# Kernel tuning notes

Measured on AMD Instinct MI355X. Metric: run time of the kernel, lower is better.

## Reference

```python
import jax, jax.numpy as jnp
import numpy as np

M = 16384      # total flat points per role (8 scenes x 2048 pts)
D = 256        # d_model
H = 4          # heads
K = 16         # knn neighbors
DFF = 1024     # 4*D
LN_EPS = 1e-5


def _ln(x, g, b):
    m = jnp.mean(x, axis=-1, keepdims=True)
    v = jnp.mean((x - m) ** 2, axis=-1, keepdims=True)
    return (x - m) / jnp.sqrt(v + LN_EPS) * g + b


def _knn_block(x, coord, ctx, ctx_coord, idx,
               Wq, Wk, Wv, Wo, g1, b1, pe_w, pe_b,
               W1, bf1, W2, bf2, g2, b2):
    # x: [M,D] query feats; ctx: [N,D] context feats; idx: [M,K] neighbor ids (-1 = invalid)
    m, d = x.shape
    k = idx.shape[1]
    dh = d // H
    valid = idx >= 0
    idx_c = jnp.where(valid, idx, 0)

    xn = _ln(x, g1, b1)
    q = (xn @ Wq).reshape(m, H, dh)                      # [M,H,dh]
    k_all = ctx @ Wk                                     # [N,D]
    v_all = ctx @ Wv                                     # [N,D]

    rel = coord[:, None, :] - ctx_coord[idx_c]           # [M,K,3]
    pe = rel @ pe_w + pe_b                               # [M,K,D] relative position encoding
    kg = (k_all[idx_c] + pe).reshape(m, k, H, dh)        # gathered keys  [M,K,H,dh]
    vg = (v_all[idx_c] + pe).reshape(m, k, H, dh)        # gathered values

    scale = jnp.asarray(1.0 / np.sqrt(dh), x.dtype)
    scores = jnp.einsum('mhd,mkhd->mhk', q, kg) * scale
    scores = jnp.where(valid[:, None, :], scores, jnp.asarray(-1e9, x.dtype))
    attn = jax.nn.softmax(scores, axis=-1)
    out = jnp.einsum('mhk,mkhd->mhd', attn, vg).reshape(m, d) @ Wo
    x = x + out
    h = jax.nn.gelu(_ln(x, g2, b2) @ W1 + bf1)
    return x + (h @ W2 + bf2)


def setup_inputs() -> dict:
    key = jax.random.key(0)
    ks = jax.random.split(key, 24)
    s = 0.02
    nblk = 2  # [0]=self(a), [1]=cross(a,b)
    inp = {
        'feat_a': jax.random.normal(ks[0], (M, D), jnp.float32),
        'coord_a': jax.random.normal(ks[1], (M, 3), jnp.float32),
        'feat_b': jax.random.normal(ks[2], (M, D), jnp.float32),
        'coord_b': jax.random.normal(ks[3], (M, 3), jnp.float32),
        'Wq': jax.random.normal(ks[4], (nblk, D, D), jnp.float32) * s,
        'Wk': jax.random.normal(ks[5], (nblk, D, D), jnp.float32) * s,
        'Wv': jax.random.normal(ks[6], (nblk, D, D), jnp.float32) * s,
        'Wo': jax.random.normal(ks[7], (nblk, D, D), jnp.float32) * s,
        'ln1_g': jnp.ones((nblk, D), jnp.float32),
        'ln1_b': jnp.zeros((nblk, D), jnp.float32),
        'pe_w': jax.random.normal(ks[8], (nblk, 3, D), jnp.float32) * s,
        'pe_b': jnp.zeros((nblk, D), jnp.float32),
        'ffn_w1': jax.random.normal(ks[9], (nblk, D, DFF), jnp.float32) * s,
        'ffn_b1': jnp.zeros((nblk, DFF), jnp.float32),
        'ffn_w2': jax.random.normal(ks[10], (nblk, DFF, D), jnp.float32) * s,
        'ffn_b2': jnp.zeros((nblk, D), jnp.float32),
        'ln2_g': jnp.ones((nblk, D), jnp.float32),
        'ln2_b': jnp.zeros((nblk, D), jnp.float32),
        'knn_a2a': jax.random.randint(ks[11], (M, K), 0, M, jnp.int64 if jax.config.jax_enable_x64 else jnp.int32),
        'knn_a2b': jax.random.randint(ks[12], (M, K), 0, M, jnp.int64 if jax.config.jax_enable_x64 else jnp.int32),
    }
    return inp


def reference(feat_a, coord_a, feat_b, coord_b,
              Wq, Wk, Wv, Wo, ln1_g, ln1_b, pe_w, pe_b,
              ffn_w1, ffn_b1, ffn_w2, ffn_b2, ln2_g, ln2_b,
              knn_a2a, knn_a2b):
    def params(i):
        return (Wq[i], Wk[i], Wv[i], Wo[i], ln1_g[i], ln1_b[i], pe_w[i], pe_b[i],
                ffn_w1[i], ffn_b1[i], ffn_w2[i], ffn_b2[i], ln2_g[i], ln2_b[i])
    # layer 'self(a)': feat[a] = block(feat[a], coord[a], knn_indexes['a2a'])
    fa = _knn_block(feat_a, coord_a, feat_a, coord_a, knn_a2a, *params(0))
    # layer 'cross(a,b)': feat[a] = block(query=feat[a], context=feat[b], knn_indexes['a2b'])
    fa = _knn_block(fa, coord_a, feat_b, coord_b, knn_a2b, *params(1))
    return fa
```

## Files before the change

### kernel.cpp

```cpp
#include <hip/hip_runtime.h>
#include <hip/hip_bf16.h>
#include <stdint.h>

#define MM 16384
#define DD 256
#define HH 4
#define KK 16
#define DFF_ 1024

typedef __attribute__((ext_vector_type(8))) short bf16x8;
typedef __attribute__((ext_vector_type(16))) float f32x16;
typedef __attribute__((ext_vector_type(2))) float f32x2;

__device__ __forceinline__ unsigned short f2bf(float f) {
    unsigned u = __builtin_bit_cast(unsigned, f);
    unsigned r = u + 0x7fffu + ((u >> 16) & 1u);
    return (unsigned short)(r >> 16);
}
__device__ __forceinline__ float bf2f(unsigned short h) {
    unsigned u = ((unsigned)h) << 16;
    return __builtin_bit_cast(float, u);
}


__global__ __launch_bounds__(256) void prep_weights(
        const float* __restrict__ Wq, const float* __restrict__ Wk,
        const float* __restrict__ Wv, const float* __restrict__ Wo,
        const float* __restrict__ W1, const float* __restrict__ W2,
        unsigned short* __restrict__ wf) {
    int t = blockIdx.x * blockDim.x + threadIdx.x;
    const float* src; unsigned short* dst;
    int kd, lg, rem, blk, e, sect;
    if (t < 131072) { sect = 0; rem = t; blk = rem >> 16; e = rem & 65535;
        src = Wq; dst = wf + blk * 65536; kd = 256; lg = 8; }
    else if (t < 262144) { sect = 1; rem = t - 131072; blk = rem >> 16; e = rem & 65535;
        src = Wk; dst = wf + 131072 + blk * 131072; kd = 256; lg = 8; }
    else if (t < 393216) { sect = 2; rem = t - 262144; blk = rem >> 16; e = rem & 65535;
        src = Wv; dst = wf + 131072 + blk * 131072; kd = 256; lg = 8; }
    else if (t < 524288) { sect = 0; rem = t - 393216; blk = rem >> 16; e = rem & 65535;
        src = Wo; dst = wf + 393216 + blk * 65536; kd = 256; lg = 8; }
    else if (t < 1048576) { sect = 0; rem = t - 524288; blk = rem >> 18; e = rem & 262143;
        src = W1; dst = wf + 524288 + blk * 262144; kd = 256; lg = 10; }
    else if (t < 1572864) { sect = 0; rem = t - 1048576; blk = rem >> 18; e = rem & 262143;
        src = W2; dst = wf + 1048576 + blk * 262144; kd = 1024; lg = 8; }
    else return;
    int k = e >> lg;
    int n = e & ((1 << lg) - 1);
    if (sect == 1) n = (n >> 2) * 8 + (n & 3);
    else if (sect == 2) n = (n >> 2) * 8 + 4 + (n & 3);
    float v = src[(size_t)blk * kd * (1 << lg) + e];
    int off = ((n >> 5) * (kd >> 4) + (k >> 4)) * 512 + (((k >> 3) & 1) * 32 + (n & 31)) * 8 + (k & 7);
    dst[off] = f2bf(v);
}

__global__ __launch_bounds__(256) void ln_to_frag(
        const float* __restrict__ x, const float* __restrict__ g,
        const float* __restrict__ b, unsigned short* __restrict__ out,
        int apply_ln) {
    int wave = threadIdx.x >> 6, lane = threadIdx.x & 63;
    int m = blockIdx.x * 4 + wave;
    const float4 xv = reinterpret_cast<const float4*>(x + (size_t)m * DD)[lane];
    float vals[4] = {xv.x, xv.y, xv.z, xv.w};
    int k0 = lane * 4;
    if (apply_ln) {
        float s = vals[0] + vals[1] + vals[2] + vals[3];
        float sq = vals[0]*vals[0] + vals[1]*vals[1] + vals[2]*vals[2] + vals[3]*vals[3];
        for (int o = 32; o; o >>= 1) { s += __shfl_xor(s, o, 64); sq += __shfl_xor(sq, o, 64); }
        float mean = s * (1.0f / DD);
        float var = sq * (1.0f / DD) - mean * mean;
        float rs = rsqrtf(var + 1e-5f);
        #pragma unroll
        for (int c = 0; c < 4; ++c)
            vals[c] = (vals[c] - mean) * rs * g[k0 + c] + b[k0 + c];
    }
    int chunk = ((m >> 5) * (DD >> 4) + (k0 >> 4)) * 64 + ((k0 >> 3) & 1) * 32 + (m & 31);
    ushort4 o4 = make_ushort4(f2bf(vals[0]), f2bf(vals[1]), f2bf(vals[2]), f2bf(vals[3]));
    *reinterpret_cast<ushort4*>(out + (size_t)chunk * 8 + (k0 & 7)) = o4;
}

constexpr int GOUT_F32 = 0;
constexpr int GOUT_GELU_FRAG = 2;

template <int KG>
__device__ __forceinline__ void compute_tile(
        const bf16x8* __restrict__ a0, const bf16x8* __restrict__ a1,
        const bf16x8* __restrict__ b0, const bf16x8* __restrict__ b1,
        f32x16 acc[2][2]) {
    #pragma unroll 4
    for (int g = 0; g < KG; ++g) {
        bf16x8 av0 = a0[g * 64];
        bf16x8 av1 = a1[g * 64];
        bf16x8 bv0 = b0[g * 64];
        bf16x8 bv1 = b1[g * 64];
        acc[0][0] = __builtin_amdgcn_mfma_f32_32x32x16_bf16(av0, bv0, acc[0][0], 0, 0, 0);
        acc[0][1] = __builtin_amdgcn_mfma_f32_32x32x16_bf16(av0, bv1, acc[0][1], 0, 0, 0);
        acc[1][0] = __builtin_amdgcn_mfma_f32_32x32x16_bf16(av1, bv0, acc[1][0], 0, 0, 0);
        acc[1][1] = __builtin_amdgcn_mfma_f32_32x32x16_bf16(av1, bv1, acc[1][1], 0, 0, 0);
    }
}

template <int KD, int NOUT, int MODE, bool RESID, bool BIAS>
__global__ __launch_bounds__(256) void gemm_frag(
        const bf16x8* __restrict__ A, const bf16x8* __restrict__ B,
        void* __restrict__ outp, const float* __restrict__ resid,
        const float* __restrict__ bias, int out_kd) {
    constexpr int KG = KD / 16;
    __shared__ float lds[MODE == GOUT_GELU_FRAG ? 4 * 1056 : 4];
    int wave = threadIdx.x >> 6, lane = threadIdx.x & 63;
    int wm = wave & 1, wn = wave >> 1;
    int m0 = blockIdx.x * 128 + wm * 64;
    int n0 = blockIdx.y * 128 + wn * 64;
    const bf16x8* a0 = A + ((size_t)(m0 >> 5) * KG) * 64 + lane;
    const bf16x8* a1 = a0 + (size_t)KG * 64;
    const bf16x8* b0 = B + ((size_t)(n0 >> 5) * KG) * 64 + lane;
    const bf16x8* b1 = b0 + (size_t)KG * 64;
    f32x16 acc[2][2] = {};
    compute_tile<KG>(a0, a1, b0, b1, acc);
    int col = lane & 31, rq = (lane >> 5) * 4;
    if constexpr (MODE == GOUT_F32) {
        #pragma unroll
        for (int i = 0; i < 2; ++i)
        #pragma unroll
        for (int j = 0; j < 2; ++j) {
            #pragma unroll
            for (int r = 0; r < 16; ++r) {
                int row = (r & 3) + 8 * (r >> 2) + rq;
                int m = m0 + i * 32 + row;
                int n = n0 + j * 32 + col;
                float v = acc[i][j][r];
                if (BIAS) v += bias[n];
                if (RESID) v += resid[(size_t)m * NOUT + n];
                ((float*)outp)[(size_t)m * NOUT + n] = v;
            }
        }
    } else {
        float* wlds = &lds[wave * 1056];
        for (int i = 0; i < 2; ++i)
        for (int j = 0; j < 2; ++j) {
            #pragma unroll
            for (int r = 0; r < 16; ++r) {
                int row = (r & 3) + 8 * (r >> 2) + rq;
                int n = n0 + j * 32 + col;
                float v = acc[i][j][r] + bias[n];
                float arg = v * (1.5957691216f + 0.0713548163f * v * v);
                v = v * __frcp_rn(1.0f + __expf(-arg));
                wlds[row * 33 + col] = v;
            }
            #pragma unroll
            for (int it = 0; it < 2; ++it) {
                int task = lane + it * 64;
                int row = task >> 2, cc = task & 3;
                int m = m0 + i * 32 + row;
                int k = n0 + j * 32 + cc * 8;
                float* p = &wlds[row * 33 + cc * 8];
                unsigned short us[8];
                #pragma unroll
                for (int e = 0; e < 8; ++e) us[e] = f2bf(p[e]);
                int chunk = ((m >> 5) * (out_kd >> 4) + (k >> 4)) * 64 + ((k >> 3) & 1) * 32 + (m & 31);
                reinterpret_cast<uint4*>(outp)[chunk] = *reinterpret_cast<uint4*>(us);
            }
        }
    }
}

__global__ __launch_bounds__(256) void gemm_qkv(
        const bf16x8* __restrict__ Aq, const bf16x8* __restrict__ Akv,
        const bf16x8* __restrict__ Bq, const bf16x8* __restrict__ Bkv,
        unsigned short* __restrict__ qout, unsigned char* __restrict__ kvout) {
    constexpr int KG = 16;
    int wave = threadIdx.x >> 6, lane = threadIdx.x & 63;
    int wm = wave & 1, wn = wave >> 1;
    int y = blockIdx.y;
    bool isQ = y < 2;
    const bf16x8* A = isQ ? Aq : Akv;
    const bf16x8* B = isQ ? Bq : Bkv;
    int n0 = (isQ ? y : y - 2) * 128 + wn * 64;
    int m0 = blockIdx.x * 128 + wm * 64;
    const bf16x8* a0 = A + ((size_t)(m0 >> 5) * KG) * 64 + lane;
    const bf16x8* a1 = a0 + (size_t)KG * 64;
    const bf16x8* b0 = B + ((size_t)(n0 >> 5) * KG) * 64 + lane;
    const bf16x8* b1 = b0 + (size_t)KG * 64;
    f32x16 acc[2][2] = {};
    compute_tile<KG>(a0, a1, b0, b1, acc);
    int col = lane & 31, rq = (lane >> 5) * 4;
    #pragma unroll
    for (int i = 0; i < 2; ++i)
    #pragma unroll
    for (int j = 0; j < 2; ++j)
    #pragma unroll
    for (int r = 0; r < 16; ++r) {
        int row = (r & 3) + 8 * (r >> 2) + rq;
        int m = m0 + i * 32 + row;
        int n = n0 + j * 32 + col;
        float v = acc[i][j][r];
        if (isQ) qout[(size_t)m * 256 + n] = f2bf(v);
        else kvout[(size_t)m * 512 + n] =
            (unsigned char)(__builtin_amdgcn_cvt_pk_fp8_f32(v, v, 0, false) & 0xff);
    }
}

__global__ __launch_bounds__(256) void attn_kernel(
        const unsigned short* __restrict__ q, const unsigned char* __restrict__ kv,
        const float* __restrict__ coord, const float* __restrict__ ctx_coord,
        const int* __restrict__ knn,
        const float* __restrict__ pe_w, const float* __restrict__ pe_b,
        unsigned short* __restrict__ out_frag) {
    int wave = threadIdx.x >> 6, lane = threadIdx.x & 63;
    int m = blockIdx.x * 4 + wave;
    int s = lane & 15;
    int d0 = (lane >> 4) * 64 + s * 4;

    ushort4 qv4 = *reinterpret_cast<const ushort4*>(q + (size_t)m * DD + d0);
    float qx = bf2f(qv4.x), qy = bf2f(qv4.y), qz = bf2f(qv4.z), qw = bf2f(qv4.w);
    float4 pw0 = *reinterpret_cast<const float4*>(pe_w + d0);
    float4 pw1 = *reinterpret_cast<const float4*>(pe_w + DD + d0);
    float4 pw2 = *reinterpret_cast<const float4*>(pe_w + 2 * DD + d0);
    float4 pbv = *reinterpret_cast<const float4*>(pe_b + d0);

    float cx = coord[m * 3], cy = coord[m * 3 + 1], cz = coord[m * 3 + 2];
    int myidx = knn[(size_t)m * KK + s];
    int icm = myidx < 0 ? 0 : myidx;
    float rx = cx - ctx_coord[icm * 3];
    float ry = cy - ctx_coord[icm * 3 + 1];
    float rz = cz - ctx_coord[icm * 3 + 2];

    float t0 = qx * pw0.x + qy * pw0.y + qz * pw0.z + qw * pw0.w;
    float t1 = qx * pw1.x + qy * pw1.y + qz * pw1.z + qw * pw1.w;
    float t2 = qx * pw2.x + qy * pw2.y + qz * pw2.z + qw * pw2.w;
    float t3 = qx * pbv.x + qy * pbv.y + qz * pbv.z + qw * pbv.w;
    #pragma unroll
    for (int o = 1; o < 16; o <<= 1) {
        t0 += __shfl_xor(t0, o, 64);
        t1 += __shfl_xor(t1, o, 64);
        t2 += __shfl_xor(t2, o, 64);
        t3 += __shfl_xor(t3, o, 64);
    }

    float sc_own = 0.0f;
    unsigned vpk[KK];
    #pragma unroll
    for (int j = 0; j < KK; ++j) {
        int ij = __shfl(myidx, j, 64);
        int ic = ij < 0 ? 0 : ij;
        uint2 kvv = *reinterpret_cast<const uint2*>(kv + (size_t)ic * 512 + (d0 >> 2) * 8);
        vpk[j] = kvv.y;
        f32x2 k01 = __builtin_amdgcn_cvt_pk_f32_fp8(kvv.x, false);
        f32x2 k23 = __builtin_amdgcn_cvt_pk_f32_fp8(kvv.x, true);
        float p = qx * k01.x + qy * k01.y + qz * k23.x + qw * k23.y;
        p += __shfl_xor(p, 1, 64);
        p += __shfl_xor(p, 2, 64);
        p += __shfl_xor(p, 4, 64);
        p += __shfl_xor(p, 8, 64);
        sc_own = (j == s) ? p : sc_own;
    }
    float corr = rx * t0 + ry * t1 + rz * t2 + t3;
    sc_own = (myidx >= 0) ? (sc_own + corr) * 0.125f : -1e9f;

    float mx = sc_own;
    mx = fmaxf(mx, __shfl_xor(mx, 1, 64));
    mx = fmaxf(mx, __shfl_xor(mx, 2, 64));
    mx = fmaxf(mx, __shfl_xor(mx, 4, 64));
    mx = fmaxf(mx, __shfl_xor(mx, 8, 64));
    float e = __expf(sc_own - mx);
    float sum = e;
    sum += __shfl_xor(sum, 1, 64);
    sum += __shfl_xor(sum, 2, 64);
    sum += __shfl_xor(sum, 4, 64);
    sum += __shfl_xor(sum, 8, 64);
    float w_own = e * __frcp_rn(sum);

    float wrx = w_own * rx, wry = w_own * ry, wrz = w_own * rz;
    #pragma unroll
    for (int o = 1; o < 16; o <<= 1) {
        wrx += __shfl_xor(wrx, o, 64);
        wry += __shfl_xor(wry, o, 64);
        wrz += __shfl_xor(wrz, o, 64);
    }

    int gbase = lane & 48;
    float ax = 0.f, ay = 0.f, az = 0.f, aw = 0.f;
    #pragma unroll
    for (int j = 0; j < KK; ++j) {
        float wj = __shfl(w_own, gbase + j, 64);
        f32x2 v01 = __builtin_amdgcn_cvt_pk_f32_fp8(vpk[j], false);
        f32x2 v23 = __builtin_amdgcn_cvt_pk_f32_fp8(vpk[j], true);
        ax += wj * v01.x;
        ay += wj * v01.y;
        az += wj * v23.x;
        aw += wj * v23.y;
    }
    ax += wrx * pw0.x + wry * pw1.x + wrz * pw2.x + pbv.x;
    ay += wrx * pw0.y + wry * pw1.y + wrz * pw2.y + pbv.y;
    az += wrx * pw0.z + wry * pw1.z + wrz * pw2.z + pbv.z;
    aw += wrx * pw0.w + wry * pw1.w + wrz * pw2.w + pbv.w;

    ushort4 o4 = make_ushort4(f2bf(ax), f2bf(ay), f2bf(az), f2bf(aw));
    int chunk = ((m >> 5) * (DD >> 4) + (d0 >> 4)) * 64 + ((d0 >> 3) & 1) * 32 + (m & 31);
    *reinterpret_cast<ushort4*>(out_frag + (size_t)chunk * 8 + (d0 & 7)) = o4;
}

extern "C" void kernel_launch(void* const* d_in, const int* in_sizes, int n_in,
                              void* d_out, int out_size, void* d_ws, size_t ws_size,
                              hipStream_t stream) {
    const float* feat_a = (const float*)d_in[0];
    const float* coord_a = (const float*)d_in[1];
    const float* feat_b = (const float*)d_in[2];
    const float* coord_b = (const float*)d_in[3];
    const float* Wq = (const float*)d_in[4];
    const float* Wk = (const float*)d_in[5];
    const float* Wv = (const float*)d_in[6];
    const float* Wo = (const float*)d_in[7];
    const float* ln1_g = (const float*)d_in[8];
    const float* ln1_b = (const float*)d_in[9];
    const float* pe_w = (const float*)d_in[10];
    const float* pe_b = (const float*)d_in[11];
    const float* W1 = (const float*)d_in[12];
    const float* b1 = (const float*)d_in[13];
    const float* W2 = (const float*)d_in[14];
    const float* b2 = (const float*)d_in[15];
    const float* ln2_g = (const float*)d_in[16];
    const float* ln2_b = (const float*)d_in[17];
    const int* knn_a2a = (const int*)d_in[18];
    const int* knn_a2b = (const int*)d_in[19];

    char* ws = (char*)d_ws;
    unsigned short* wfrag = (unsigned short*)ws;
    float* xmid = (float*)(ws + (4ull << 20));
    float* xout0 = (float*)(ws + (20ull << 20));
    unsigned short* qbuf = (unsigned short*)(ws + (36ull << 20));
    unsigned char* kvbuf = (unsigned char*)(ws + (52ull << 20));
    unsigned short* xnf = (unsigned short*)(ws + (68ull << 20));
    unsigned short* ctxf = (unsigned short*)(ws + (76ull << 20));
    unsigned short* attnf = (unsigned short*)(ws + (84ull << 20));
    unsigned short* geluf = (unsigned short*)(ws + (36ull << 20));

    const unsigned short* WQF = wfrag;
    const unsigned short* KVF = wfrag + 131072;
    const unsigned short* WOF = wfrag + 393216;
    const unsigned short* W1F = wfrag + 524288;
    const unsigned short* W2F = wfrag + 1048576;

    prep_weights<<<(1572864 + 255) / 256, 256, 0, stream>>>(Wq, Wk, Wv, Wo, W1, W2, wfrag);

    for (int blk = 0; blk < 2; ++blk) {
        const float* x_in = blk ? xout0 : feat_a;
        const float* ctx = blk ? feat_b : feat_a;
        const float* ccrd = blk ? coord_b : coord_a;
        const int* knn = blk ? knn_a2b : knn_a2a;
        float* x_out_final = blk ? (float*)d_out : xout0;

        ln_to_frag<<<MM / 4, 256, 0, stream>>>(ctx, nullptr, nullptr, ctxf, 0);
        ln_to_frag<<<MM / 4, 256, 0, stream>>>(x_in, ln1_g + blk * DD, ln1_b + blk * DD, xnf, 1);

        gemm_qkv<<<dim3(MM / 128, 6), 256, 0, stream>>>(
            (const bf16x8*)xnf, (const bf16x8*)ctxf,
            (const bf16x8*)(WQF + blk * 65536), (const bf16x8*)(KVF + blk * 131072),
            qbuf, kvbuf);

        attn_kernel<<<MM / 4, 256, 0, stream>>>(qbuf, kvbuf, coord_a, ccrd, knn,
                                                pe_w + blk * 3 * DD, pe_b + blk * DD, attnf);

        gemm_frag<256, 256, GOUT_F32, true, false><<<dim3(MM / 128, 2), 256, 0, stream>>>(
            (const bf16x8*)attnf, (const bf16x8*)(WOF + blk * 65536), xmid, x_in, nullptr, 0);

        ln_to_frag<<<MM / 4, 256, 0, stream>>>(xmid, ln2_g + blk * DD, ln2_b + blk * DD, xnf, 1);

        gemm_frag<256, 1024, GOUT_GELU_FRAG, false, true><<<dim3(MM / 128, 8), 256, 0, stream>>>(
            (const bf16x8*)xnf, (const bf16x8*)(W1F + blk * 262144), geluf, nullptr,
            b1 + blk * DFF_, 1024);

        gemm_frag<1024, 256, GOUT_F32, true, true><<<dim3(MM / 128, 2), 256, 0, stream>>>(
            (const bf16x8*)geluf, (const bf16x8*)(W2F + blk * 262144), x_out_final, xmid,
            b2 + blk * DD, 0);
    }
}
```

Baseline: 349.1 us.

## Fuse LayerNorm into residual GEMM epilogues and batch input fragment conversion

Adds a gemm_ln kernel that computes a full 256-column row tile per block (64 rows × 4 waves). It adds bias and residual, writes the fp32 result, then reduces row statistics across waves to emit the next LayerNorm as bf16 fragments. This removes the separate ln_to_frag passes after the Wo projection and after the first FFN. A single 3-way launch prepares LN1(feat_a), ctx_a and ctx_b fragments up front. The cost is lower grid parallelism on those GEMMs (256 blocks instead of 256×2 tiles) and heavier epilogue register and LDS use.

```diff
diff --git a/kernel.cpp b/kernel.cpp
--- a/kernel.cpp
+++ b/kernel.cpp
@@ -53,10 +53,15 @@
     dst[off] = f2bf(v);
 }
 
-__global__ __launch_bounds__(256) void ln_to_frag(
-        const float* __restrict__ x, const float* __restrict__ g,
-        const float* __restrict__ b, unsigned short* __restrict__ out,
-        int apply_ln) {
+__global__ __launch_bounds__(256) void ln3_to_frag(
+        const float* __restrict__ xa, const float* __restrict__ g,
+        const float* __restrict__ b, const float* __restrict__ xb,
+        unsigned short* __restrict__ outln, unsigned short* __restrict__ outca,
+        unsigned short* __restrict__ outcb) {
+    int y = blockIdx.y;
+    const float* x = (y == 2) ? xb : xa;
+    unsigned short* out = (y == 0) ? outln : (y == 1 ? outca : outcb);
+    int apply_ln = (y == 0);
     int wave = threadIdx.x >> 6, lane = threadIdx.x & 63;
     int m = blockIdx.x * 4 + wave;
     const float4 xv = reinterpret_cast<const float4*>(x + (size_t)m * DD)[lane];
@@ -163,6 +168,141 @@
     }
 }
 
+template <int O, int N>
+__device__ __forceinline__ void redstage(float* a, int lane) {
+    int sel = lane & O;
+    #pragma unroll
+    for (int u = 0; u < N / 2; ++u) {
+        float lo = a[2 * u], hi = a[2 * u + 1];
+        float keep = sel ? hi : lo;
+        float send = sel ? lo : hi;
+        a[u] = keep + __shfl_xor(send, O, 64);
+    }
+}
+
+template <int KD, bool BIAS>
+__global__ __launch_bounds__(256) void gemm_ln(
+        const bf16x8* __restrict__ A, const bf16x8* __restrict__ B,
+        float* __restrict__ out_f32, const float* __restrict__ resid,
+        const float* __restrict__ bias,
+        const float* __restrict__ lng, const float* __restrict__ lnb,
+        unsigned short* __restrict__ out_frag) {
+    constexpr int KG = KD / 16;
+    __shared__ float pstat[4][64][2];
+    __shared__ float stats[64][2];
+    __shared__ float tlds[4][32 * 33];
+    int wave = threadIdx.x >> 6, lane = threadIdx.x & 63;
+    int wn = wave;
+    int m0 = blockIdx.x * 64;
+    int n0 = wn * 64;
+    const bf16x8* a0 = A + ((size_t)(m0 >> 5) * KG) * 64 + lane;
+    const bf16x8* a1 = a0 + (size_t)KG * 64;
+    const bf16x8* b0 = B + ((size_t)(n0 >> 5) * KG) * 64 + lane;
+    const bf16x8* b1 = b0 + (size_t)KG * 64;
+    f32x16 acc[2][2] = {};
+    compute_tile<KG>(a0, a1, b0, b1, acc);
+    int col = lane & 31, rq = (lane >> 5) * 4;
+
+    #pragma unroll
+    for (int i = 0; i < 2; ++i)
+    #pragma unroll
+    for (int j = 0; j < 2; ++j) {
+        #pragma unroll
+        for (int r = 0; r < 16; ++r) {
+            int row = (r & 3) + 8 * (r >> 2) + rq;
+            int m = m0 + i * 32 + row;
+            int n = n0 + j * 32 + col;
+            float v = acc[i][j][r];
+            if (BIAS) v += bias[n];
+            v += resid[(size_t)m * DD + n];
+            out_f32[(size_t)m * DD + n] = v;
+            acc[i][j][r] = v;
+        }
+    }
+
+    {
+        float ps[32];
+        #pragma unroll
+        for (int i = 0; i < 2; ++i)
+        #pragma unroll
+        for (int r = 0; r < 16; ++r)
+            ps[i * 16 + r] = acc[i][0][r] + acc[i][1][r];
+        redstage<1, 32>(ps, lane);
+        redstage<2, 16>(ps, lane);
+        redstage<4, 8>(ps, lane);
+        redstage<8, 4>(ps, lane);
+        redstage<16, 2>(ps, lane);
+        float sum64 = ps[0];
+        float qs[32];
+        #pragma unroll
+        for (int i = 0; i < 2; ++i)
+        #pragma unroll
+        for (int r = 0; r < 16; ++r) {
+            float a = acc[i][0][r], b = acc[i][1][r];
+            qs[i * 16 + r] = a * a + b * b;
+        }
+        redstage<1, 32>(qs, lane);
+        redstage<2, 16>(qs, lane);
+        redstage<4, 8>(qs, lane);
+        redstage<8, 4>(qs, lane);
+        redstage<16, 2>(qs, lane);
+        float sq64 = qs[0];
+        int slot = lane & 31;
+        int ROW = (slot >> 4) * 32 + (slot & 3) + 8 * ((slot >> 2) & 3) + rq;
+        *reinterpret_cast<float2*>(&pstat[wn][ROW][0]) = make_float2(sum64, sq64);
+    }
+    __syncthreads();
+    if (threadIdx.x < 64) {
+        int R = threadIdx.x;
+        float s = 0.0f, sq = 0.0f;
+        #pragma unroll
+        for (int w = 0; w < 4; ++w) {
+            float2 p = *reinterpret_cast<float2*>(&pstat[w][R][0]);
+            s += p.x; sq += p.y;
+        }
+        float mean = s * (1.0f / DD);
+        float var = sq * (1.0f / DD) - mean * mean;
+        float rstd = rsqrtf(var + 1e-5f);
+        *reinterpret_cast<float2*>(&stats[R][0]) = make_float2(mean, rstd);
+    }
+    __syncthreads();
+
+    float* wlds = &tlds[wave][0];
+    #pragma unroll
+    for (int i = 0; i < 2; ++i) {
+        float mean_r[16], rstd_r[16];
+        #pragma unroll
+        for (int r = 0; r < 16; ++r) {
+            int row = (r & 3) + 8 * (r >> 2) + rq;
+            float2 st = *reinterpret_cast<float2*>(&stats[i * 32 + row][0]);
+            mean_r[r] = st.x; rstd_r[r] = st.y;
+        }
+        for (int j = 0; j < 2; ++j) {
+            float gj = lng[n0 + j * 32 + col];
+            float bj = lnb[n0 + j * 32 + col];
+            #pragma unroll
+            for (int r = 0; r < 16; ++r) {
+                int row = (r & 3) + 8 * (r >> 2) + rq;
+                float v = (acc[i][j][r] - mean_r[r]) * rstd_r[r] * gj + bj;
+                wlds[row * 33 + col] = v;
+            }
+            #pragma unroll
+            for (int it = 0; it < 2; ++it) {
+                int task = lane + it * 64;
+                int row = task >> 2, cc = task & 3;
+                int m = m0 + i * 32 + row;
+                int k = n0 + j * 32 + cc * 8;
+                float* p = &wlds[row * 33 + cc * 8];
+                unsigned short us[8];
+                #pragma unroll
+                for (int e = 0; e < 8; ++e) us[e] = f2bf(p[e]);
+                int chunk = ((m >> 5) * (DD >> 4) + (k >> 4)) * 64 + ((k >> 3) & 1) * 32 + (m & 31);
+                *reinterpret_cast<uint4*>(out_frag + (size_t)chunk * 8) = *reinterpret_cast<uint4*>(us);
+            }
+        }
+    }
+}
+
 __global__ __launch_bounds__(256) void gemm_qkv(
         const bf16x8* __restrict__ Aq, const bf16x8* __restrict__ Akv,
         const bf16x8* __restrict__ Bq, const bf16x8* __restrict__ Bkv,
@@ -330,8 +470,9 @@
     unsigned short* qbuf = (unsigned short*)(ws + (36ull << 20));
     unsigned char* kvbuf = (unsigned char*)(ws + (52ull << 20));
     unsigned short* xnf = (unsigned short*)(ws + (68ull << 20));
-    unsigned short* ctxf = (unsigned short*)(ws + (76ull << 20));
+    unsigned short* ctxfa = (unsigned short*)(ws + (76ull << 20));
     unsigned short* attnf = (unsigned short*)(ws + (84ull << 20));
+    unsigned short* ctxfb = (unsigned short*)(ws + (92ull << 20));
     unsigned short* geluf = (unsigned short*)(ws + (36ull << 20));
 
     const unsigned short* WQF = wfrag;
@@ -342,35 +483,43 @@
 
     prep_weights<<<(1572864 + 255) / 256, 256, 0, stream>>>(Wq, Wk, Wv, Wo, W1, W2, wfrag);
 
-    for (int blk = 0; blk < 2; ++blk) {
-        const float* x_in = blk ? xout0 : feat_a;
-        const float* ctx = blk ? feat_b : feat_a;
-        const float* ccrd = blk ? coord_b : coord_a;
-        const int* knn = blk ? knn_a2b : knn_a2a;
-        float* x_out_final = blk ? (float*)d_out : xout0;
-
-        ln_to_frag<<<MM / 4, 256, 0, stream>>>(ctx, nullptr, nullptr, ctxf, 0);
-        ln_to_frag<<<MM / 4, 256, 0, stream>>>(x_in, ln1_g + blk * DD, ln1_b + blk * DD, xnf, 1);
-
-        gemm_qkv<<<dim3(MM / 128, 6), 256, 0, stream>>>(
-            (const bf16x8*)xnf, (const bf16x8*)ctxf,
-            (const bf16x8*)(WQF + blk * 65536), (const bf16x8*)(KVF + blk * 131072),
-            qbuf, kvbuf);
-
-        attn_kernel<<<MM / 4, 256, 0, stream>>>(qbuf, kvbuf, coord_a, ccrd, knn,
-                                                pe_w + blk * 3 * DD, pe_b + blk * DD, attnf);
-
-        gemm_frag<256, 256, GOUT_F32, true, false><<<dim3(MM / 128, 2), 256, 0, stream>>>(
-            (const bf16x8*)attnf, (const bf16x8*)(WOF + blk * 65536), xmid, x_in, nullptr, 0);
-
-        ln_to_frag<<<MM / 4, 256, 0, stream>>>(xmid, ln2_g + blk * DD, ln2_b + blk * DD, xnf, 1);
-
-        gemm_frag<256, 1024, GOUT_GELU_FRAG, false, true><<<dim3(MM / 128, 8), 256, 0, stream>>>(
-            (const bf16x8*)xnf, (const bf16x8*)(W1F + blk * 262144), geluf, nullptr,
-            b1 + blk * DFF_, 1024);
-
-        gemm_frag<1024, 256, GOUT_F32, true, true><<<dim3(MM / 128, 2), 256, 0, stream>>>(
-            (const bf16x8*)geluf, (const bf16x8*)(W2F + blk * 262144), x_out_final, xmid,
-            b2 + blk * DD, 0);
-    }
-}
+    ln3_to_frag<<<dim3(MM / 4, 3), 256, 0, stream>>>(feat_a, ln1_g, ln1_b, feat_b,
+                                                     xnf, ctxfa, ctxfb);
+
+    gemm_qkv<<<dim3(MM / 128, 6), 256, 0, stream>>>(
+        (const bf16x8*)xnf, (const bf16x8*)ctxfa,
+        (const bf16x8*)WQF, (const bf16x8*)KVF, qbuf, kvbuf);
+
+    attn_kernel<<<MM / 4, 256, 0, stream>>>(qbuf, kvbuf, coord_a, coord_a, knn_a2a,
+                                            pe_w, pe_b, attnf);
+
+    gemm_ln<256, false><<<MM / 64, 256, 0, stream>>>(
+        (const bf16x8*)attnf, (const bf16x8*)WOF, xmid, feat_a, nullptr,
+        ln2_g, ln2_b, xnf);
+
+    gemm_frag<256, 1024, GOUT_GELU_FRAG, false, true><<<dim3(MM / 128, 8), 256, 0, stream>>>(
+        (const bf16x8*)xnf, (const bf16x8*)W1F, geluf, nullptr, b1, 1024);
+
+    gemm_ln<1024, true><<<MM / 64, 256, 0, stream>>>(
+        (const bf16x8*)geluf, (const bf16x8*)W2F, xout0, xmid, b2,
+        ln1_g + DD, ln1_b + DD, xnf);
+
+    gemm_qkv<<<dim3(MM / 128, 6), 256, 0, stream>>>(
+        (const bf16x8*)xnf, (const bf16x8*)ctxfb,
+        (const bf16x8*)(WQF + 65536), (const bf16x8*)(KVF + 131072), qbuf, kvbuf);
+
+    attn_kernel<<<MM / 4, 256, 0, stream>>>(qbuf, kvbuf, coord_a, coord_b, knn_a2b,
+                                            pe_w + 3 * DD, pe_b + DD, attnf);
+
+    gemm_ln<256, false><<<MM / 64, 256, 0, stream>>>(
+        (const bf16x8*)attnf, (const bf16x8*)(WOF + 65536), xmid, xout0, nullptr,
+        ln2_g + DD, ln2_b + DD, xnf);
+
+    gemm_frag<256, 1024, GOUT_GELU_FRAG, false, true><<<dim3(MM / 128, 8), 256, 0, stream>>>(
+        (const bf16x8*)xnf, (const bf16x8*)(W1F + 262144), geluf, nullptr,
+        b1 + DFF_, 1024);
+
+    gemm_frag<1024, 256, GOUT_F32, true, true><<<dim3(MM / 128, 2), 256, 0, stream>>>(
+        (const bf16x8*)geluf, (const bf16x8*)(W2F + 262144), d_out, xmid,
+        b2 + DD, 0);
+}
```

Result: faster. 335.7 us (-3.8%).
